# Kernel tuning notes

Measured on AMD Instinct MI355X. Metric: run time of the kernel, lower is better.

The kernel has to match this reference:

```python
import jax, jax.numpy as jnp
import numpy as np

N = 100000   # nodes
E = 600000   # edges
V = 64       # vocab
D = 128      # emb_dim
H = 128      # hidden_dim
G = 256      # graphs in batch


def setup_inputs():
    key = jax.random.key(0)
    ks = jax.random.split(key, 12)
    x_idx = jax.random.randint(ks[0], (N,), 0, V)
    edge_index = jax.random.randint(ks[1], (2, E), 0, N)
    batch = jnp.sort(jax.random.randint(ks[2], (N,), 0, G))
    emb = jax.random.normal(ks[3], (V, D), jnp.float32) * 0.02
    emb = emb.at[0].set(0.0)  # padding_idx=0
    def lin(k, o, i):
        return jax.random.normal(k, (o, i), jnp.float32) * (1.0 / np.sqrt(i))
    return dict(
        x_idx=x_idx, edge_index=edge_index, batch=batch, emb=emb,
        ln0_g=jnp.ones((D,), jnp.float32), ln0_b=jnp.zeros((D,), jnp.float32),
        w0_l=lin(ks[4], H, D), b0_l=jnp.zeros((H,), jnp.float32), w0_r=lin(ks[5], H, D),
        ln1_g=jnp.ones((H,), jnp.float32), ln1_b=jnp.zeros((H,), jnp.float32),
        w1_l=lin(ks[6], H, H), b1_l=jnp.zeros((H,), jnp.float32), w1_r=lin(ks[7], H, H),
        mlp_w1=lin(ks[8], H // 2, H), mlp_b1=jnp.zeros((H // 2,), jnp.float32),
        mlp_w2=lin(ks[9], 2, H // 2), mlp_b2=jnp.zeros((2,), jnp.float32),
    )


def _layernorm(x, g, b, eps=1e-5):
    m = jnp.mean(x, axis=-1, keepdims=True)
    v = jnp.var(x, axis=-1, keepdims=True)
    return (x - m) * jax.lax.rsqrt(v + eps) * g + b


def _sage_conv(x, src, dst, w_l, b_l, w_r):
    # PyG SAGEConv (mean aggr): out = lin_l(mean_{j->i} x_j) + lin_r(x_i)
    agg = jax.ops.segment_sum(x[src], dst, num_segments=N)        # [N, F]
    deg = jax.ops.segment_sum(jnp.ones((src.shape[0],), x.dtype), dst, num_segments=N)
    agg = agg / jnp.maximum(deg, 1.0)[:, None]
    return agg @ w_l.T + b_l + x @ w_r.T


def reference(x_idx, edge_index, batch, emb,
              ln0_g, ln0_b, w0_l, b0_l, w0_r,
              ln1_g, ln1_b, w1_l, b1_l, w1_r,
              mlp_w1, mlp_b1, mlp_w2, mlp_b2):
    src, dst = edge_index[0], edge_index[1]
    x = emb[x_idx]                                   # [N, D]
    # layer 0 (dropout is identity in eval mode)
    x = _layernorm(x, ln0_g, ln0_b)
    x = jax.nn.relu(_sage_conv(x, src, dst, w0_l, b0_l, w0_r))
    # layer 1
    x = _layernorm(x, ln1_g, ln1_b)
    x = jax.nn.relu(_sage_conv(x, src, dst, w1_l, b1_l, w1_r))
    # global mean pool over graphs
    sums = jax.ops.segment_sum(x, batch, num_segments=G)          # [G, H]
    cnts = jax.ops.segment_sum(jnp.ones((N,), x.dtype), batch, num_segments=G)
    g = sums / jnp.maximum(cnts, 1.0)[:, None]
    # MLP head
    h = jax.nn.relu(g @ mlp_w1.T + mlp_b1)
    return h @ mlp_w2.T + mlp_b2                                   # [G, 2]
```

## Files before the change

kernel.cpp:

```cpp
#include <hip/hip_runtime.h>

#define NN 100000
#define NE 600000
#define DIM 128
#define NG 256
#define NB_SCAN 391

typedef __attribute__((ext_vector_type(8))) short short8_t;
typedef __attribute__((ext_vector_type(4))) float f32x4;

__device__ __forceinline__ ushort f2bf(float f) {
  unsigned u = __float_as_uint(f);
  unsigned r = (u + 0x7fffu + ((u >> 16) & 1u)) >> 16;
  return (ushort)r;
}
__device__ __forceinline__ float bf2f(ushort h) {
  return __uint_as_float(((unsigned)h) << 16);
}

__global__ __launch_bounds__(256) void embed_ln_kernel(
    const int* __restrict__ x_idx, const float* __restrict__ emb,
    const float* __restrict__ g, const float* __restrict__ b,
    float* __restrict__ out) {
  int wave = threadIdx.x >> 6;
  int lane = threadIdx.x & 63;
  int n = blockIdx.x * 4 + wave;
  if (n >= NN) return;
  int idx = x_idx[n];
  float2 v = ((const float2*)(emb + (size_t)idx * DIM))[lane];
  float s = v.x + v.y;
  float sq = v.x * v.x + v.y * v.y;
  for (int off = 32; off; off >>= 1) {
    s += __shfl_xor(s, off);
    sq += __shfl_xor(sq, off);
  }
  float m = s * (1.0f / 128.0f);
  float var = sq * (1.0f / 128.0f) - m * m;
  float r = rsqrtf(var + 1e-5f);
  float2 gg = ((const float2*)g)[lane];
  float2 bb = ((const float2*)b)[lane];
  float2 o;
  o.x = (v.x - m) * r * gg.x + bb.x;
  o.y = (v.y - m) * r * gg.y + bb.y;
  ((float2*)(out + (size_t)n * DIM))[lane] = o;
}

__global__ __launch_bounds__(256) void ln_kernel(
    const float* __restrict__ in, const float* __restrict__ g,
    const float* __restrict__ b, float* __restrict__ out) {
  int wave = threadIdx.x >> 6;
  int lane = threadIdx.x & 63;
  int n = blockIdx.x * 4 + wave;
  if (n >= NN) return;
  float2 v = ((const float2*)(in + (size_t)n * DIM))[lane];
  float s = v.x + v.y;
  float sq = v.x * v.x + v.y * v.y;
  for (int off = 32; off; off >>= 1) {
    s += __shfl_xor(s, off);
    sq += __shfl_xor(sq, off);
  }
  float m = s * (1.0f / 128.0f);
  float var = sq * (1.0f / 128.0f) - m * m;
  float r = rsqrtf(var + 1e-5f);
  float2 gg = ((const float2*)g)[lane];
  float2 bb = ((const float2*)b)[lane];
  float2 o;
  o.x = (v.x - m) * r * gg.x + bb.x;
  o.y = (v.y - m) * r * gg.y + bb.y;
  ((float2*)(out + (size_t)n * DIM))[lane] = o;
}

__global__ __launch_bounds__(256) void deg_int_kernel(const int* __restrict__ dst,
                                                      int* __restrict__ degi) {
  int e = blockIdx.x * 256 + threadIdx.x;
  if (e < NE) atomicAdd(degi + dst[e], 1);
}

__global__ __launch_bounds__(256) void scan1_kernel(const int* __restrict__ degi,
                                                    int* __restrict__ excl,
                                                    int* __restrict__ bsum) {
  __shared__ int tmp[256];
  int t = threadIdx.x;
  int i = blockIdx.x * 256 + t;
  int v = (i < NN) ? degi[i] : 0;
  int val = v;
  tmp[t] = val;
  __syncthreads();
  for (int off = 1; off < 256; off <<= 1) {
    int add = (t >= off) ? tmp[t - off] : 0;
    __syncthreads();
    val += add;
    tmp[t] = val;
    __syncthreads();
  }
  if (i < NN) excl[i] = val - v;
  if (t == 255) bsum[blockIdx.x] = val;
}

__global__ __launch_bounds__(512) void scan2_kernel(int* __restrict__ bsum,
                                                    int* __restrict__ bscan) {
  __shared__ int tmp[512];
  int t = threadIdx.x;
  int v = (t < NB_SCAN) ? bsum[t] : 0;
  int val = v;
  tmp[t] = val;
  __syncthreads();
  for (int off = 1; off < 512; off <<= 1) {
    int add = (t >= off) ? tmp[t - off] : 0;
    __syncthreads();
    val += add;
    tmp[t] = val;
    __syncthreads();
  }
  if (t < NB_SCAN) bscan[t] = val - v;
}

__global__ __launch_bounds__(256) void scan3_kernel(const int* __restrict__ excl,
                                                    const int* __restrict__ bscan,
                                                    int* __restrict__ row_off,
                                                    int* __restrict__ cursor) {
  int i = blockIdx.x * 256 + threadIdx.x;
  if (i < NN) {
    int r = excl[i] + bscan[i >> 8];
    row_off[i] = r;
    cursor[i] = r;
  }
  if (i == 0) row_off[NN] = NE;
}

__global__ __launch_bounds__(256) void fill_kernel(const int* __restrict__ src,
                                                   const int* __restrict__ dst,
                                                   int* __restrict__ cursor,
                                                   int* __restrict__ csr_src) {
  int e = blockIdx.x * 256 + threadIdx.x;
  if (e < NE) {
    int d = dst[e];
    int slot = atomicAdd(cursor + d, 1);
    csr_src[slot] = src[e];
  }
}

__global__ __launch_bounds__(256) void gather_mean_kernel(
    const int* __restrict__ row_off, const int* __restrict__ csr_src,
    const float* __restrict__ x, float* __restrict__ agg) {
  int t = threadIdx.x;
  int q = t & 31;
  int node = blockIdx.x * 8 + (t >> 5);
  if (node >= NN) return;
  int beg = row_off[node], end = row_off[node + 1];
  float4 acc = make_float4(0.f, 0.f, 0.f, 0.f);
  for (int e = beg; e < end; ++e) {
    int s = csr_src[e];
    float4 v = ((const float4*)(x + (size_t)s * DIM))[q];
    acc.x += v.x; acc.y += v.y; acc.z += v.z; acc.w += v.w;
  }
  float sc = 1.0f / fmaxf((float)(end - beg), 1.0f);
  acc.x *= sc; acc.y *= sc; acc.z *= sc; acc.w *= sc;
  ((float4*)(agg + (size_t)node * DIM))[q] = acc;
}

__global__ __launch_bounds__(256) void prep_w_kernel(const float* __restrict__ wl,
                                                     const float* __restrict__ wr,
                                                     ushort* __restrict__ wp) {
  int t = blockIdx.x * 256 + threadIdx.x;
  int e = t & 7;
  int lane = (t >> 3) & 63;
  int ht = (t >> 9) & 7;
  int j = (t >> 12) & 1;
  int p = (t >> 13) & 3;
  int h = ht * 16 + (lane & 15);
  int lq = lane >> 4;
  int k = p * 64 + j * 32 + lq * 4 + (e & 3) + 16 * (e >> 2);
  float v = (k < 128) ? wl[h * 128 + k] : wr[h * 128 + (k - 128)];
  ushort hi = f2bf(v);
  ushort lo = f2bf(v - bf2f(hi));
  wp[(((p * 2 + 0) * 2 + j) * 8 + ht) * 512 + lane * 8 + e] = hi;
  wp[(((p * 2 + 1) * 2 + j) * 8 + ht) * 512 + lane * 8 + e] = lo;
}

__global__ __launch_bounds__(256, 2) void conv_mfma_kernel(
    const float* __restrict__ xln, const float* __restrict__ agg,
    const ushort* __restrict__ wp, const float* __restrict__ bl,
    float* __restrict__ out) {
  __shared__ ushort Xs[2][128 * 64];
  __shared__ ushort Wl[16384];
  const int t = threadIdx.x;
  const int lane = t & 63;
  const int wv = t >> 6;
  const int l15 = lane & 15;
  const int lq = lane >> 4;
  const int nbase = blockIdx.x * 128;

  f32x4 acc[2][8];
#pragma unroll
  for (int a = 0; a < 2; ++a)
#pragma unroll
    for (int b = 0; b < 8; ++b) acc[a][b] = (f32x4){0.f, 0.f, 0.f, 0.f};

  const int srow = t >> 1;
  const int sh2 = t & 1;
  const int gn_s = nbase + srow;
  const bool sval = gn_s < NN;
  char* lds_hi = (char*)&Xs[0][0];
  char* lds_lo = (char*)&Xs[1][0];
  const int sswz = (srow & 7) << 4;

  for (int p = 0; p < 4; ++p) {
    const float* srcp = (p < 2) ? agg : xln;
    const int kb = (p & 1) * 64;
    {
      const ushort* wsrc = wp + p * 16384;
#pragma unroll
      for (int i = 0; i < 8; ++i)
        *(short8_t*)(Wl + i * 2048 + t * 8) = *(const short8_t*)(wsrc + i * 2048 + t * 8);
    }
#pragma unroll
    for (int i = 0; i < 8; ++i) {
      int qd = sh2 * 8 + i;
      float4 v = make_float4(0.f, 0.f, 0.f, 0.f);
      if (sval) v = *(const float4*)(srcp + (size_t)gn_s * DIM + kb + qd * 4);
      int j = qd >> 3;
      int a = qd & 7;
      int inner = j * 64 + ((a < 4) ? a * 16 : (a - 4) * 16 + 8);
      int off = srow * 128 + inner;
      ushort4 hi, lo;
      hi.x = f2bf(v.x); lo.x = f2bf(v.x - bf2f(hi.x));
      hi.y = f2bf(v.y); lo.y = f2bf(v.y - bf2f(hi.y));
      hi.z = f2bf(v.z); lo.z = f2bf(v.z - bf2f(hi.z));
      hi.w = f2bf(v.w); lo.w = f2bf(v.w - bf2f(hi.w));
      *(ushort4*)(lds_hi + (off ^ sswz)) = hi;
      *(ushort4*)(lds_lo + (off ^ sswz)) = lo;
    }
    __syncthreads();
#pragma unroll
    for (int j = 0; j < 2; ++j) {
      short8_t ahi[2], alo[2];
#pragma unroll
      for (int nt = 0; nt < 2; ++nt) {
        int row = wv * 32 + nt * 16 + l15;
        int off = row * 128 + j * 64 + lq * 16;
        int sw = (row & 7) << 4;
        ahi[nt] = *(short8_t*)(lds_hi + (off ^ sw));
        alo[nt] = *(short8_t*)(lds_lo + (off ^ sw));
      }
#pragma unroll
      for (int ht = 0; ht < 8; ++ht) {
        short8_t bhi = *(const short8_t*)(Wl + ((0 * 2 + j) * 8 + ht) * 512 + lane * 8);
        short8_t blo = *(const short8_t*)(Wl + ((1 * 2 + j) * 8 + ht) * 512 + lane * 8);
        acc[0][ht] = __builtin_amdgcn_mfma_f32_16x16x32_bf16(ahi[0], bhi, acc[0][ht], 0, 0, 0);
        acc[1][ht] = __builtin_amdgcn_mfma_f32_16x16x32_bf16(ahi[1], bhi, acc[1][ht], 0, 0, 0);
        acc[0][ht] = __builtin_amdgcn_mfma_f32_16x16x32_bf16(alo[0], bhi, acc[0][ht], 0, 0, 0);
        acc[1][ht] = __builtin_amdgcn_mfma_f32_16x16x32_bf16(alo[1], bhi, acc[1][ht], 0, 0, 0);
        acc[0][ht] = __builtin_amdgcn_mfma_f32_16x16x32_bf16(ahi[0], blo, acc[0][ht], 0, 0, 0);
        acc[1][ht] = __builtin_amdgcn_mfma_f32_16x16x32_bf16(ahi[1], blo, acc[1][ht], 0, 0, 0);
      }
    }
    __syncthreads();
  }
#pragma unroll
  for (int ht = 0; ht < 8; ++ht) {
    float bv = bl[ht * 16 + l15];
#pragma unroll
    for (int nt = 0; nt < 2; ++nt) {
#pragma unroll
      for (int r = 0; r < 4; ++r) {
        int node = nbase + wv * 32 + nt * 16 + lq * 4 + r;
        if (node < NN)
          out[(size_t)node * DIM + ht * 16 + l15] = fmaxf(acc[nt][ht][r] + bv, 0.f);
      }
    }
  }
}

#define PCHUNK 128
__global__ __launch_bounds__(128) void pool_kernel(const float* __restrict__ x,
                                                   const int* __restrict__ batch,
                                                   float* __restrict__ pool,
                                                   float* __restrict__ cnt) {
  int f = threadIdx.x;
  int n0 = blockIdx.x * PCHUNK;
  float acc = 0.f;
  int cur = batch[n0];
  int runlen = 0;
  for (int i = 0; i < PCHUNK; ++i) {
    int n = n0 + i;
    if (n >= NN) break;
    int bg = batch[n];
    if (bg != cur) {
      atomicAdd(&pool[cur * DIM + f], acc);
      if (f == 0) atomicAdd(&cnt[cur], (float)runlen);
      acc = 0.f;
      runlen = 0;
      cur = bg;
    }
    acc += x[(size_t)n * DIM + f];
    runlen++;
  }
  if (runlen > 0) {
    atomicAdd(&pool[cur * DIM + f], acc);
    if (f == 0) atomicAdd(&cnt[cur], (float)runlen);
  }
}

__global__ __launch_bounds__(128) void head_kernel(
    const float* __restrict__ pool, const float* __restrict__ cnt,
    const float* __restrict__ w1, const float* __restrict__ b1,
    const float* __restrict__ w2, const float* __restrict__ b2,
    float* __restrict__ out) {
  __shared__ float gsh[128];
  __shared__ float h[64];
  int g = blockIdx.x;
  int t = threadIdx.x;
  float ic = 1.0f / fmaxf(cnt[g], 1.0f);
  gsh[t] = pool[g * DIM + t] * ic;
  __syncthreads();
  if (t < 64) {
    float a = b1[t];
#pragma unroll 8
    for (int k = 0; k < 128; ++k) a += gsh[k] * w1[t * 128 + k];
    h[t] = fmaxf(a, 0.f);
  }
  __syncthreads();
  if (t < 2) {
    float a = b2[t];
#pragma unroll
    for (int k = 0; k < 64; ++k) a += h[k] * w2[t * 64 + k];
    out[g * 2 + t] = a;
  }
}

extern "C" void kernel_launch(void* const* d_in, const int* in_sizes, int n_in,
                              void* d_out, int out_size, void* d_ws, size_t ws_size,
                              hipStream_t stream) {
  const int* x_idx = (const int*)d_in[0];
  const int* eidx = (const int*)d_in[1];
  const int* batch = (const int*)d_in[2];
  const float* emb = (const float*)d_in[3];
  const float* ln0g = (const float*)d_in[4];
  const float* ln0b = (const float*)d_in[5];
  const float* w0l = (const float*)d_in[6];
  const float* b0l = (const float*)d_in[7];
  const float* w0r = (const float*)d_in[8];
  const float* ln1g = (const float*)d_in[9];
  const float* ln1b = (const float*)d_in[10];
  const float* w1l = (const float*)d_in[11];
  const float* b1l = (const float*)d_in[12];
  const float* w1r = (const float*)d_in[13];
  const float* mw1 = (const float*)d_in[14];
  const float* mb1 = (const float*)d_in[15];
  const float* mw2 = (const float*)d_in[16];
  const float* mb2 = (const float*)d_in[17];
  float* out = (float*)d_out;

  float* ws = (float*)d_ws;
  float* x = ws;
  float* agg = x + (size_t)NN * DIM;
  float* pool = agg + (size_t)NN * DIM;
  float* cnt = pool + (size_t)NG * DIM;
  ushort* wp0 = (ushort*)(cnt + NG);
  ushort* wp1 = wp0 + 65536;
  int* degi = (int*)(wp1 + 65536);
  int* excl = degi + NN;
  int* row_off = excl + NN;
  int* cursor = row_off + NN + 1;
  int* bsum = cursor + NN;
  int* bscan = bsum + 512;
  int* csr_src = bscan + 512;

  const int* src = eidx;
  const int* dst = eidx + NE;

  hipMemsetAsync(pool, 0, ((size_t)NG * DIM + NG) * sizeof(float), stream);
  hipMemsetAsync(degi, 0, (size_t)NN * sizeof(int), stream);

  deg_int_kernel<<<(NE + 255) / 256, 256, 0, stream>>>(dst, degi);
  scan1_kernel<<<NB_SCAN, 256, 0, stream>>>(degi, excl, bsum);
  scan2_kernel<<<1, 512, 0, stream>>>(bsum, bscan);
  scan3_kernel<<<NB_SCAN, 256, 0, stream>>>(excl, bscan, row_off, cursor);
  fill_kernel<<<(NE + 255) / 256, 256, 0, stream>>>(src, dst, cursor, csr_src);

  prep_w_kernel<<<128, 256, 0, stream>>>(w0l, w0r, wp0);
  prep_w_kernel<<<128, 256, 0, stream>>>(w1l, w1r, wp1);

  embed_ln_kernel<<<NN / 4, 256, 0, stream>>>(x_idx, emb, ln0g, ln0b, x);

  gather_mean_kernel<<<(NN + 7) / 8, 256, 0, stream>>>(row_off, csr_src, x, agg);
  conv_mfma_kernel<<<(NN + 127) / 128, 256, 0, stream>>>(x, agg, wp0, b0l, agg);
  ln_kernel<<<NN / 4, 256, 0, stream>>>(agg, ln1g, ln1b, x);
  gather_mean_kernel<<<(NN + 7) / 8, 256, 0, stream>>>(row_off, csr_src, x, agg);
  conv_mfma_kernel<<<(NN + 127) / 128, 256, 0, stream>>>(x, agg, wp1, b1l, agg);

  pool_kernel<<<(NN + PCHUNK - 1) / PCHUNK, 128, 0, stream>>>(agg, batch, pool, cnt);
  head_kernel<<<NG, 128, 0, stream>>>(pool, cnt, mw1, mb1, mw2, mb2, out);
}
```

Before: 475.0 us.

## Fuse layernorm into conv epilogue and emit MFMA-ready bf16 split aggregates

The gather kernel now writes the mean aggregate already split into bf16 hi/lo and laid out as MFMA A-fragments. The conv kernel can therefore load those fragments straight from global memory instead of staging and converting fp32 data through LDS. The second layer's layernorm moves into the first conv's epilogue, which removes the separate ln_kernel and one full read/write pass over the node features. Weights are now read directly from global memory instead of LDS, and the LDS saving allows three blocks per CU. The trade-off is more global and L1 weight traffic and more register pressure from the fused LN epilogue.

```diff
diff --git a/kernel.cpp b/kernel.cpp
--- a/kernel.cpp
+++ b/kernel.cpp
@@ -4,6 +4,7 @@
 #define NE 600000
 #define DIM 128
 #define NG 256
+#define NGRP 6250
 #define NB_SCAN 391
 
 typedef __attribute__((ext_vector_type(8))) short short8_t;
@@ -28,31 +29,6 @@
   if (n >= NN) return;
   int idx = x_idx[n];
   float2 v = ((const float2*)(emb + (size_t)idx * DIM))[lane];
-  float s = v.x + v.y;
-  float sq = v.x * v.x + v.y * v.y;
-  for (int off = 32; off; off >>= 1) {
-    s += __shfl_xor(s, off);
-    sq += __shfl_xor(sq, off);
-  }
-  float m = s * (1.0f / 128.0f);
-  float var = sq * (1.0f / 128.0f) - m * m;
-  float r = rsqrtf(var + 1e-5f);
-  float2 gg = ((const float2*)g)[lane];
-  float2 bb = ((const float2*)b)[lane];
-  float2 o;
-  o.x = (v.x - m) * r * gg.x + bb.x;
-  o.y = (v.y - m) * r * gg.y + bb.y;
-  ((float2*)(out + (size_t)n * DIM))[lane] = o;
-}
-
-__global__ __launch_bounds__(256) void ln_kernel(
-    const float* __restrict__ in, const float* __restrict__ g,
-    const float* __restrict__ b, float* __restrict__ out) {
-  int wave = threadIdx.x >> 6;
-  int lane = threadIdx.x & 63;
-  int n = blockIdx.x * 4 + wave;
-  if (n >= NN) return;
-  float2 v = ((const float2*)(in + (size_t)n * DIM))[lane];
   float s = v.x + v.y;
   float sq = v.x * v.x + v.y * v.y;
   for (int off = 32; off; off >>= 1) {
@@ -142,7 +118,7 @@
 
 __global__ __launch_bounds__(256) void gather_mean_kernel(
     const int* __restrict__ row_off, const int* __restrict__ csr_src,
-    const float* __restrict__ x, float* __restrict__ agg) {
+    const float* __restrict__ x, ushort* __restrict__ af) {
   int t = threadIdx.x;
   int q = t & 31;
   int node = blockIdx.x * 8 + (t >> 5);
@@ -156,7 +132,16 @@
   }
   float sc = 1.0f / fmaxf((float)(end - beg), 1.0f);
   acc.x *= sc; acc.y *= sc; acc.z *= sc; acc.w *= sc;
-  ((float4*)(agg + (size_t)node * DIM))[q] = acc;
+  ushort4 hi, lo;
+  hi.x = f2bf(acc.x); lo.x = f2bf(acc.x - bf2f(hi.x));
+  hi.y = f2bf(acc.y); lo.y = f2bf(acc.y - bf2f(hi.y));
+  hi.z = f2bf(acc.z); lo.z = f2bf(acc.z - bf2f(hi.z));
+  hi.w = f2bf(acc.w); lo.w = f2bf(acc.w - bf2f(hi.w));
+  int g = node >> 4, l15n = node & 15;
+  int jb = q >> 3, lqw = q & 3, ebase = q & 4;
+  size_t base = (((size_t)g * 4 + jb) * 64 + lqw * 16 + l15n) * 16;
+  *(ushort4*)(af + base + ebase) = hi;
+  *(ushort4*)(af + base + 8 + ebase) = lo;
 }
 
 __global__ __launch_bounds__(256) void prep_w_kernel(const float* __restrict__ wl,
@@ -178,12 +163,12 @@
   wp[(((p * 2 + 1) * 2 + j) * 8 + ht) * 512 + lane * 8 + e] = lo;
 }
 
-__global__ __launch_bounds__(256, 2) void conv_mfma_kernel(
-    const float* __restrict__ xln, const float* __restrict__ agg,
+__global__ __launch_bounds__(256, 3) void conv_mfma_kernel(
+    const float* __restrict__ xln, const ushort* __restrict__ af,
     const ushort* __restrict__ wp, const float* __restrict__ bl,
-    float* __restrict__ out) {
+    const float* __restrict__ lng, const float* __restrict__ lnb,
+    float* __restrict__ out, int do_ln) {
   __shared__ ushort Xs[2][128 * 64];
-  __shared__ ushort Wl[16384];
   const int t = threadIdx.x;
   const int lane = t & 63;
   const int wv = t >> 6;
@@ -205,20 +190,15 @@
   char* lds_lo = (char*)&Xs[1][0];
   const int sswz = (srow & 7) << 4;
 
-  for (int p = 0; p < 4; ++p) {
-    const float* srcp = (p < 2) ? agg : xln;
-    const int kb = (p & 1) * 64;
-    {
-      const ushort* wsrc = wp + p * 16384;
-#pragma unroll
-      for (int i = 0; i < 8; ++i)
-        *(short8_t*)(Wl + i * 2048 + t * 8) = *(const short8_t*)(wsrc + i * 2048 + t * 8);
-    }
+#pragma unroll 1
+  for (int ph = 0; ph < 2; ++ph) {
+    if (ph) __syncthreads();
+    const int kb = ph * 64;
 #pragma unroll
     for (int i = 0; i < 8; ++i) {
       int qd = sh2 * 8 + i;
       float4 v = make_float4(0.f, 0.f, 0.f, 0.f);
-      if (sval) v = *(const float4*)(srcp + (size_t)gn_s * DIM + kb + qd * 4);
+      if (sval) v = *(const float4*)(xln + (size_t)gn_s * DIM + kb + qd * 4);
       int j = qd >> 3;
       int a = qd & 7;
       int inner = j * 64 + ((a < 4) ? a * 16 : (a - 4) * 16 + 8);
@@ -232,6 +212,7 @@
       *(ushort4*)(lds_lo + (off ^ sswz)) = lo;
     }
     __syncthreads();
+    const int pk = ph + 2;
 #pragma unroll
     for (int j = 0; j < 2; ++j) {
       short8_t ahi[2], alo[2];
@@ -245,8 +226,8 @@
       }
 #pragma unroll
       for (int ht = 0; ht < 8; ++ht) {
-        short8_t bhi = *(const short8_t*)(Wl + ((0 * 2 + j) * 8 + ht) * 512 + lane * 8);
-        short8_t blo = *(const short8_t*)(Wl + ((1 * 2 + j) * 8 + ht) * 512 + lane * 8);
+        short8_t bhi = *(const short8_t*)(wp + (((pk * 2 + 0) * 2 + j) * 8 + ht) * 512 + lane * 8);
+        short8_t blo = *(const short8_t*)(wp + (((pk * 2 + 1) * 2 + j) * 8 + ht) * 512 + lane * 8);
         acc[0][ht] = __builtin_amdgcn_mfma_f32_16x16x32_bf16(ahi[0], bhi, acc[0][ht], 0, 0, 0);
         acc[1][ht] = __builtin_amdgcn_mfma_f32_16x16x32_bf16(ahi[1], bhi, acc[1][ht], 0, 0, 0);
         acc[0][ht] = __builtin_amdgcn_mfma_f32_16x16x32_bf16(alo[0], bhi, acc[0][ht], 0, 0, 0);
@@ -255,18 +236,96 @@
         acc[1][ht] = __builtin_amdgcn_mfma_f32_16x16x32_bf16(ahi[1], blo, acc[1][ht], 0, 0, 0);
       }
     }
-    __syncthreads();
-  }
+  }
+
+  const int gblk = blockIdx.x * 8 + wv * 2;
+#pragma unroll 1
+  for (int ph = 2; ph < 4; ++ph) {
+    const int pk = ph - 2;
+#pragma unroll
+    for (int j = 0; j < 2; ++j) {
+      int jb = (ph & 1) * 2 + j;
+      short8_t ahi[2], alo[2];
+#pragma unroll
+      for (int nt = 0; nt < 2; ++nt) {
+        int g = gblk + nt;
+        if (g < NGRP) {
+          size_t base = (((size_t)g * 4 + jb) * 64 + lane) * 16;
+          ahi[nt] = *(const short8_t*)(af + base);
+          alo[nt] = *(const short8_t*)(af + base + 8);
+        } else {
+          ahi[nt] = (short8_t){0, 0, 0, 0, 0, 0, 0, 0};
+          alo[nt] = (short8_t){0, 0, 0, 0, 0, 0, 0, 0};
+        }
+      }
+#pragma unroll
+      for (int ht = 0; ht < 8; ++ht) {
+        short8_t bhi = *(const short8_t*)(wp + (((pk * 2 + 0) * 2 + j) * 8 + ht) * 512 + lane * 8);
+        short8_t blo = *(const short8_t*)(wp + (((pk * 2 + 1) * 2 + j) * 8 + ht) * 512 + lane * 8);
+        acc[0][ht] = __builtin_amdgcn_mfma_f32_16x16x32_bf16(ahi[0], bhi, acc[0][ht], 0, 0, 0);
+        acc[1][ht] = __builtin_amdgcn_mfma_f32_16x16x32_bf16(ahi[1], bhi, acc[1][ht], 0, 0, 0);
+        acc[0][ht] = __builtin_amdgcn_mfma_f32_16x16x32_bf16(alo[0], bhi, acc[0][ht], 0, 0, 0);
+        acc[1][ht] = __builtin_amdgcn_mfma_f32_16x16x32_bf16(alo[1], bhi, acc[1][ht], 0, 0, 0);
+        acc[0][ht] = __builtin_amdgcn_mfma_f32_16x16x32_bf16(ahi[0], blo, acc[0][ht], 0, 0, 0);
+        acc[1][ht] = __builtin_amdgcn_mfma_f32_16x16x32_bf16(ahi[1], blo, acc[1][ht], 0, 0, 0);
+      }
+    }
+  }
+
 #pragma unroll
   for (int ht = 0; ht < 8; ++ht) {
     float bv = bl[ht * 16 + l15];
 #pragma unroll
+    for (int nt = 0; nt < 2; ++nt)
+#pragma unroll
+      for (int r = 0; r < 4; ++r) acc[nt][ht][r] = fmaxf(acc[nt][ht][r] + bv, 0.f);
+  }
+  if (do_ln) {
+    float gg[8], bb[8];
+#pragma unroll
+    for (int ht = 0; ht < 8; ++ht) {
+      gg[ht] = lng[ht * 16 + l15];
+      bb[ht] = lnb[ht * 16 + l15];
+    }
+#pragma unroll
+    for (int nt = 0; nt < 2; ++nt) {
+#pragma unroll
+      for (int r = 0; r < 4; ++r) {
+        float s = 0.f, sq = 0.f;
+#pragma unroll
+        for (int ht = 0; ht < 8; ++ht) {
+          float v = acc[nt][ht][r];
+          s += v;
+          sq += v * v;
+        }
+#pragma unroll
+        for (int msk = 1; msk < 16; msk <<= 1) {
+          s += __shfl_xor(s, msk);
+          sq += __shfl_xor(sq, msk);
+        }
+        float m = s * (1.0f / 128.0f);
+        float var = sq * (1.0f / 128.0f) - m * m;
+        float rstd = rsqrtf(var + 1e-5f);
+        int node = nbase + wv * 32 + nt * 16 + lq * 4 + r;
+        if (node < NN) {
+#pragma unroll
+          for (int ht = 0; ht < 8; ++ht)
+            out[(size_t)node * DIM + ht * 16 + l15] =
+                (acc[nt][ht][r] - m) * rstd * gg[ht] + bb[ht];
+        }
+      }
+    }
+  } else {
+#pragma unroll
     for (int nt = 0; nt < 2; ++nt) {
 #pragma unroll
       for (int r = 0; r < 4; ++r) {
         int node = nbase + wv * 32 + nt * 16 + lq * 4 + r;
-        if (node < NN)
-          out[(size_t)node * DIM + ht * 16 + l15] = fmaxf(acc[nt][ht][r] + bv, 0.f);
+        if (node < NN) {
+#pragma unroll
+          for (int ht = 0; ht < 8; ++ht)
+            out[(size_t)node * DIM + ht * 16 + l15] = acc[nt][ht][r];
+        }
       }
     }
   }
@@ -354,8 +413,8 @@
 
   float* ws = (float*)d_ws;
   float* x = ws;
-  float* agg = x + (size_t)NN * DIM;
-  float* pool = agg + (size_t)NN * DIM;
+  ushort* af = (ushort*)(x + (size_t)NN * DIM);
+  float* pool = (float*)(af + (size_t)NN * DIM * 2);
   float* cnt = pool + (size_t)NG * DIM;
   ushort* wp0 = (ushort*)(cnt + NG);
   ushort* wp1 = wp0 + 65536;
@@ -384,12 +443,11 @@
 
   embed_ln_kernel<<<NN / 4, 256, 0, stream>>>(x_idx, emb, ln0g, ln0b, x);
 
-  gather_mean_kernel<<<(NN + 7) / 8, 256, 0, stream>>>(row_off, csr_src, x, agg);
-  conv_mfma_kernel<<<(NN + 127) / 128, 256, 0, stream>>>(x, agg, wp0, b0l, agg);
-  ln_kernel<<<NN / 4, 256, 0, stream>>>(agg, ln1g, ln1b, x);
-  gather_mean_kernel<<<(NN + 7) / 8, 256, 0, stream>>>(row_off, csr_src, x, agg);
-  conv_mfma_kernel<<<(NN + 127) / 128, 256, 0, stream>>>(x, agg, wp1, b1l, agg);
-
-  pool_kernel<<<(NN + PCHUNK - 1) / PCHUNK, 128, 0, stream>>>(agg, batch, pool, cnt);
+  gather_mean_kernel<<<(NN + 7) / 8, 256, 0, stream>>>(row_off, csr_src, x, af);
+  conv_mfma_kernel<<<(NN + 127) / 128, 256, 0, stream>>>(x, af, wp0, b0l, ln1g, ln1b, x, 1);
+  gather_mean_kernel<<<(NN + 7) / 8, 256, 0, stream>>>(row_off, csr_src, x, af);
+  conv_mfma_kernel<<<(NN + 127) / 128, 256, 0, stream>>>(x, af, wp1, b1l, (const float*)0, (const float*)0, x, 0);
+
+  pool_kernel<<<(NN + PCHUNK - 1) / PCHUNK, 128, 0, stream>>>(x, batch, pool, cnt);
   head_kernel<<<NG, 128, 0, stream>>>(pool, cnt, mw1, mb1, mw2, mb2, out);
 }
```

Result: faster. 461.0 us (-3.0%).
